# Kernel tuning notes

Measured on AMD Instinct MI355X. Metric: run time of the kernel, lower is better.

Reference implementation:

```python
import jax, jax.numpy as jnp
import numpy as np

NEG_SLOPE = 0.2
MASK_FILL = -1e9


def setup_inputs() -> dict:
    key = jax.random.key(0)
    k1, k2, k3, k4 = jax.random.split(key, 4)
    B, N, IN_DIM = 4, 2048, 256
    H, D = 8, 64  # n_heads, hidden_dim (out_dim)
    nodes = jax.random.normal(k1, (B, N, IN_DIM), dtype=jnp.float32)
    edges = jax.random.randint(k2, (B, N, N), 0, 2, dtype=jnp.int32)
    # Xavier-uniform-ish init for params
    pw_lim = float(np.sqrt(6.0 / (IN_DIM + H * D)))
    proj_weights = jax.random.uniform(k3, (IN_DIM, H * D), dtype=jnp.float32,
                                      minval=-pw_lim, maxval=pw_lim)
    aw_lim = float(np.sqrt(6.0 / (H + 2 * D)))
    attn_weights = jax.random.uniform(k4, (H, 2 * D), dtype=jnp.float32,
                                      minval=-aw_lim, maxval=aw_lim)
    return {"nodes": nodes, "edges": edges,
            "proj_weights": proj_weights, "attn_weights": attn_weights}


def reference(nodes, edges, proj_weights, attn_weights):
    B, N, _ = nodes.shape
    H, twoD = attn_weights.shape
    D = twoD // 2
    # Projection: [B,N,in] @ [in,H*D] -> [B,H,N,D]
    mapped = jnp.matmul(nodes, proj_weights).reshape(B, N, H, D).transpose(0, 2, 1, 3)
    # The left@diag(a)@right^T trick is exactly a_l.h_i + a_r.h_j:
    a_l = attn_weights[:, :D]   # [H,D]
    a_r = attn_weights[:, D:]   # [H,D]
    el = jnp.einsum('bhnd,hd->bhn', mapped, a_l)  # score contribution of source i
    er = jnp.einsum('bhnd,hd->bhn', mapped, a_r)  # score contribution of target j
    scores = jax.nn.leaky_relu(el[:, :, :, None] + er[:, :, None, :],
                               negative_slope=NEG_SLOPE)  # [B,H,N,N]
    scores = jnp.where(edges[:, None, :, :] == 0, MASK_FILL, scores)
    attn = jax.nn.softmax(scores, axis=-1)  # dropout p=0 -> identity
    out = jnp.einsum('bhij,bhjd->bhid', attn, mapped)  # [B,H,N,D]
    out = out.transpose(0, 2, 1, 3).reshape(B, N, H * D)  # is_concat=True
    return jax.nn.sigmoid(out)
```

## Files before the change

kernel.cpp:

```cpp
#include <hip/hip_runtime.h>
#include <hip/hip_fp16.h>
#include <math.h>

#define NEG 0.2f
#define LOG2E 1.4426950408889634f

typedef float f32x4 __attribute__((ext_vector_type(4)));
typedef _Float16 half8 __attribute__((ext_vector_type(8)));
typedef _Float16 h2v __attribute__((ext_vector_type(2)));
typedef short s16x2 __attribute__((ext_vector_type(2)));

#if __has_builtin(__builtin_amdgcn_exp2f)
#define EXP2F(x) __builtin_amdgcn_exp2f(x)
#else
#define EXP2F(x) exp2f(x)
#endif

__device__ inline uint cvt2(float a, float b) {
  union {
    decltype(__builtin_amdgcn_cvt_pkrtz(0.f, 0.f)) v;
    uint u;
  } x;
  x.v = __builtin_amdgcn_cvt_pkrtz(a, b);
  return x.u;
}

__device__ inline h2v u2h(uint u) {
  union {
    uint u;
    h2v v;
  } x;
  x.u = u;
  return x.v;
}

__device__ inline uint h2u(h2v v) {
  union {
    uint u;
    h2v v;
  } x;
  x.v = v;
  return x.u;
}

__device__ inline uint sgn16(uint t) {
  union {
    uint u;
    s16x2 v;
  } x;
  x.u = t;
  x.v = x.v >> 15;
  return x.u;
}


__global__ __launch_bounds__(256, 4) void prep_pack(
    const float* __restrict__ W, ushort* __restrict__ wf, uint* __restrict__ ermx,
    const int* __restrict__ e, uint* __restrict__ epk32) {
  const int bx = blockIdx.x;
  const int t = threadIdx.x;
  const int l = t & 63;
  if (bx < 33) {
    if (bx == 32) {
      if (t < 32) ermx[t] = 0u;
      return;
    }
    const int h = bx >> 2, ct = bx & 3;
#pragma unroll
    for (int s = 0; s < 2; ++s) {
      int slot = t + s * 256;
      int ll = slot & 63, kk = slot >> 6;
      int col = h * 64 + ct * 16 + (ll & 15);
      int k0 = kk * 32 + (ll >> 4) * 8;
      uint outv[4];
#pragma unroll
      for (int c = 0; c < 4; ++c) {
        float x0 = W[(size_t)(k0 + 2 * c) * 512 + col];
        float x1 = W[(size_t)(k0 + 2 * c + 1) * 512 + col];
        outv[c] = cvt2(x0, x1);
      }
      *(uint4*)&wf[(((size_t)((h * 4 + ct) * 8 + kk)) * 64 + ll) * 8] = *(uint4*)outv;
    }
    return;
  }
  const size_t g0 = (size_t)(bx - 33) * 16 + (t >> 6) * 4;
#pragma unroll
  for (int it = 0; it < 4; ++it) {
    const size_t gi = g0 + it;
    int4 v = *(const int4*)(e + gi * 256 + l * 4);
    unsigned long long b0 = __ballot(v.x != 0);
    unsigned long long b1 = __ballot(v.y != 0);
    unsigned long long b2 = __ballot(v.z != 0);
    unsigned long long b3 = __ballot(v.w != 0);
    if (l == 0) {
      uint4 lo, hi;
      lo.x = (uint)b0;
      lo.y = (uint)b1;
      lo.z = (uint)b2;
      lo.w = (uint)b3;
      hi.x = (uint)(b0 >> 32);
      hi.y = (uint)(b1 >> 32);
      hi.z = (uint)(b2 >> 32);
      hi.w = (uint)(b3 >> 32);
      *(uint4*)&epk32[gi * 8] = lo;
      *(uint4*)&epk32[gi * 8 + 4] = hi;
    }
  }
}

__global__ __launch_bounds__(256, 4) void pack2_proj(
    const int* __restrict__ e, uint* __restrict__ epk32,
    const float* __restrict__ A, const ushort* __restrict__ wf,
    const float* __restrict__ aw, ushort* __restrict__ mt,
    float* __restrict__ el, float* __restrict__ er, uint* __restrict__ ermx) {
  __shared__ ushort ct_lds[64][72];
  const int bx = blockIdx.x;
  const int t = threadIdx.x;
  const int l = t & 63;
  if (bx % 3 != 2) {
    const int pb = (bx / 3) * 2 + (bx % 3);
    const size_t g0 = 32768 + (size_t)pb * 16 + (t >> 6) * 4;
#pragma unroll
    for (int it = 0; it < 4; ++it) {
      const size_t gi = g0 + it;
      int4 v = *(const int4*)(e + gi * 256 + l * 4);
      unsigned long long b0 = __ballot(v.x != 0);
      unsigned long long b1 = __ballot(v.y != 0);
      unsigned long long b2 = __ballot(v.z != 0);
      unsigned long long b3 = __ballot(v.w != 0);
      if (l == 0) {
        uint4 lo, hi;
        lo.x = (uint)b0;
        lo.y = (uint)b1;
        lo.z = (uint)b2;
        lo.w = (uint)b3;
        hi.x = (uint)(b0 >> 32);
        hi.y = (uint)(b1 >> 32);
        hi.z = (uint)(b2 >> 32);
        hi.w = (uint)(b3 >> 32);
        *(uint4*)&epk32[gi * 8] = lo;
        *(uint4*)&epk32[gi * 8 + 4] = hi;
      }
    }
    return;
  }
  const int pid = bx / 3;
  const int wq = t >> 6;
  const int i0 = (pid & 127) * 64;
  const int h = pid >> 7;
  const int b = i0 >> 11, n0 = i0 & 2047, bh = b * 8 + h;
  const int cl = l & 15, hi = l >> 4;
  const float* arow = A + (size_t)(i0 + wq * 16 + cl) * 256 + hi * 8;
  const int4* wfb = (const int4*)wf + (size_t)h * 32 * 64 + l;
  f32x4 acc[4];
#pragma unroll
  for (int ct = 0; ct < 4; ++ct) acc[ct] = (f32x4){0.f, 0.f, 0.f, 0.f};
#pragma unroll
  for (int kk = 0; kk < 8; ++kk) {
    float4 a0 = *(const float4*)(arow + kk * 32);
    float4 a1 = *(const float4*)(arow + kk * 32 + 4);
    union {
      uint u[4];
      half8 v;
    } af;
    af.u[0] = cvt2(a0.x, a0.y);
    af.u[1] = cvt2(a0.z, a0.w);
    af.u[2] = cvt2(a1.x, a1.y);
    af.u[3] = cvt2(a1.z, a1.w);
#pragma unroll
    for (int ct = 0; ct < 4; ++ct) {
      union {
        int4 i;
        half8 v;
      } bf;
      bf.i = wfb[((size_t)ct * 8 + kk) * 64];
      acc[ct] = __builtin_amdgcn_mfma_f32_16x16x32_f16(af.v, bf.v, acc[ct], 0, 0, 0);
    }
  }
  float alc[4], arc[4];
#pragma unroll
  for (int ct = 0; ct < 4; ++ct) {
    alc[ct] = aw[h * 128 + ct * 16 + cl];
    arc[ct] = aw[h * 128 + 64 + ct * 16 + cl];
  }
  float ermax_loc = -1e30f;
#pragma unroll
  for (int reg = 0; reg < 4; ++reg) {
    float pl = acc[0][reg] * alc[0] + acc[1][reg] * alc[1] + acc[2][reg] * alc[2] +
               acc[3][reg] * alc[3];
    float pr = acc[0][reg] * arc[0] + acc[1][reg] * arc[1] + acc[2][reg] * arc[2] +
               acc[3][reg] * arc[3];
#pragma unroll
    for (int s = 1; s < 16; s <<= 1) {
      pl += __shfl_xor(pl, s);
      pr += __shfl_xor(pr, s);
    }
    if (cl == 0) {
      int n = n0 + wq * 16 + hi * 4 + reg;
      el[(size_t)bh * 2048 + n] = pl;
      er[(size_t)bh * 2048 + n] = pr;
    }
    ermax_loc = fmaxf(ermax_loc, pr);
  }
  ermax_loc = fmaxf(ermax_loc, __shfl_xor(ermax_loc, 16));
  ermax_loc = fmaxf(ermax_loc, __shfl_xor(ermax_loc, 32));
  if (l == 0) {
    uint bits = __float_as_uint(ermax_loc);
    uint key = (bits & 0x80000000u) ? ~bits : (bits | 0x80000000u);
    atomicMax(&ermx[bh], key);
  }
#pragma unroll
  for (int ct = 0; ct < 4; ++ct) {
    ushort4 us;
    us.x = __half_as_ushort(__float2half(acc[ct][0]));
    us.y = __half_as_ushort(__float2half(acc[ct][1]));
    us.z = __half_as_ushort(__float2half(acc[ct][2]));
    us.w = __half_as_ushort(__float2half(acc[ct][3]));
    *(ushort4*)&ct_lds[ct * 16 + cl][wq * 16 + hi * 4] = us;
  }
  __syncthreads();
  {
    const int f = t >> 5, s = t & 31;
    const int g = f >> 2, nt = f & 3;
    const int r = nt * 16 + (s & 15);
    const int cm = g * 32 + (s >> 4) * 8;
    int4 v0 = *(const int4*)&ct_lds[r][cm];
    int4 v1 = *(const int4*)&ct_lds[r][cm + 16];
    const size_t base = ((size_t)bh * 32 + (n0 >> 6)) * 4096 + f * 512;
    *(int4*)&mt[base + s * 8] = v0;
    *(int4*)&mt[base + (s + 32) * 8] = v1;
  }
}

__global__ __launch_bounds__(512, 4) void gat_attn(
    const ushort* __restrict__ mt, const uint* __restrict__ epk32,
    const float* __restrict__ el, const float* __restrict__ er,
    const uint* __restrict__ ermx, float* __restrict__ out) {
  __shared__ __align__(16) char smem[40960];
  int4* vt4 = (int4*)smem;
  uint* ysh = (uint*)(smem + 32768);
  uint* vsh = (uint*)(smem + 36864);
  const int t = threadIdx.x;
  const int l = t & 63;
  const int hf = t >> 8;
  const int th = t & 255;
  const int wq = (t >> 6) & 3;
  const int r16 = l & 15, hi = l >> 4;
  const int i0 = blockIdx.x * 64;
  const int h = blockIdx.y, b = blockIdx.z;
  const int bh = b * 8 + h;
  const uint ky = ermx[bh];
  const float emx = __uint_as_float((ky & 0x80000000u) ? (ky ^ 0x80000000u) : ~ky);
  {
    float4 e0 = *(const float4*)&er[(size_t)bh * 2048 + t * 4];
    uint2 yp, vp;
    yp.x = cvt2(EXP2F((e0.x - emx) * LOG2E), EXP2F((e0.y - emx) * LOG2E));
    yp.y = cvt2(EXP2F((e0.z - emx) * LOG2E), EXP2F((e0.w - emx) * LOG2E));
    vp.x = cvt2(EXP2F((e0.x - emx) * (NEG * LOG2E)), EXP2F((e0.y - emx) * (NEG * LOG2E)));
    vp.y = cvt2(EXP2F((e0.z - emx) * (NEG * LOG2E)), EXP2F((e0.w - emx) * (NEG * LOG2E)));
    *(uint2*)&ysh[t * 2] = yp;
    *(uint2*)&vsh[t * 2] = vp;
  }
  const int irow = i0 + wq * 16 + r16;
  h2v X2, U2;
  {
    const float s0 = el[(size_t)bh * 2048 + irow] + emx;
    const float m2 = fmaxf(s0, NEG * s0) * LOG2E;
    const float Xf = EXP2F(s0 * LOG2E - m2);
    const float Uf = EXP2F(NEG * s0 * LOG2E - m2);
    X2 = u2h(cvt2(Xf, Xf));
    U2 = u2h(cvt2(Uf, Uf));
  }
  const uint* prow = epk32 + (size_t)(b * 2048 + irow) * 64 + hf * 32;
  f32x4 acc[4];
  f32x4 accL = {0.f, 0.f, 0.f, 0.f};
#pragma unroll
  for (int nt = 0; nt < 4; ++nt) acc[nt] = (f32x4){0.f, 0.f, 0.f, 0.f};
  half8 ones;
#pragma unroll
  for (int c = 0; c < 8; ++c) ones[c] = (_Float16)1.f;

  const int4* srcbase = (const int4*)mt + ((size_t)bh * 32 + hf * 16) * 512 + wq * 128 + l;
  uint4 epw = *(const uint4*)&prow[0];
  {
    int4 p0 = srcbase[0];
    int4 p1 = srcbase[64];
    int4* d = vt4 + hf * 512 + wq * 128 + l;
    d[0] = p0;
    d[64] = p1;
  }
  __syncthreads();
  int cur = 0;
  for (int jt = 0; jt < 16; ++jt) {
    int4 nx0, nx1;
    uint4 epwn;
    if (jt < 15) {
      const int4* s = srcbase + (size_t)(jt + 1) * 512;
      nx0 = s[0];
      nx1 = s[64];
      const int jn = jt + 1;
      epwn = *(const uint4*)&prow[((jn >> 2) << 3) + (((jn >> 1) & 1) << 2)];
    }
    half8 af[2];
#pragma unroll
    for (int g = 0; g < 2; ++g) {
      const uint idx = (hf * 16 + jt) * 32 + g * 16 + hi * 4;
      uint4 y4 = *(const uint4*)&ysh[idx];
      uint4 v4 = *(const uint4*)&vsh[idx];
      const uint bsh = ((jt & 1) << 4) + (g << 3) + hi * 2;
      const uint p0 = epw.x >> bsh, p1 = epw.y >> bsh;
      const uint p2 = epw.z >> bsh, p3 = epw.w >> bsh;
      union {
        uint u[4];
        half8 v8;
      } fr;
      fr.u[0] = h2u(__builtin_elementwise_max(X2 * u2h(y4.x), U2 * u2h(v4.x))) &
                sgn16(((p0 & 1u) << 15) | (p1 << 31));
      fr.u[1] = h2u(__builtin_elementwise_max(X2 * u2h(y4.y), U2 * u2h(v4.y))) &
                sgn16(((p2 & 1u) << 15) | (p3 << 31));
      fr.u[2] = h2u(__builtin_elementwise_max(X2 * u2h(y4.z), U2 * u2h(v4.z))) &
                sgn16((((p0 >> 1) & 1u) << 15) | ((p1 >> 1) << 31));
      fr.u[3] = h2u(__builtin_elementwise_max(X2 * u2h(y4.w), U2 * u2h(v4.w))) &
                sgn16((((p2 >> 1) & 1u) << 15) | ((p3 >> 1) << 31));
      af[g] = fr.v8;
    }
    const half8* fb = (const half8*)(vt4 + cur * 1024 + hf * 512);
    __builtin_amdgcn_s_setprio(1);
#pragma unroll
    for (int g = 0; g < 2; ++g) {
      accL = __builtin_amdgcn_mfma_f32_16x16x32_f16(af[g], ones, accL, 0, 0, 0);
#pragma unroll
      for (int nt = 0; nt < 4; ++nt) {
        half8 bfr = fb[(g * 4 + nt) * 64 + l];
        acc[nt] = __builtin_amdgcn_mfma_f32_16x16x32_f16(af[g], bfr, acc[nt], 0, 0, 0);
      }
    }
    __builtin_amdgcn_s_setprio(0);
    if (jt < 15) {
      int4* d = vt4 + (cur ^ 1) * 1024 + hf * 512 + wq * 128 + l;
      d[0] = nx0;
      d[64] = nx1;
      epw = epwn;
    }
    __syncthreads();
    cur ^= 1;
  }
  float* red = (float*)smem;
  if (hf == 1) {
    float* dst = red + th * 21;
#pragma unroll
    for (int nt = 0; nt < 4; ++nt)
#pragma unroll
      for (int k = 0; k < 4; ++k) dst[nt * 4 + k] = acc[nt][k];
#pragma unroll
    for (int k = 0; k < 4; ++k) dst[16 + k] = accL[k];
  }
  __syncthreads();
  if (hf == 0) {
    const float* src = red + th * 21;
#pragma unroll
    for (int reg = 0; reg < 4; ++reg) {
      float Lrow = accL[reg] + src[16 + reg];
      float invL = 1.f / Lrow;
      int orow = i0 + wq * 16 + hi * 4 + reg;
#pragma unroll
      for (int nt = 0; nt < 4; ++nt) {
        float o = (acc[nt][reg] + src[nt * 4 + reg]) * invL;
        float sig = 1.f / (1.f + __expf(-o));
        out[(size_t)(b * 2048 + orow) * 512 + h * 64 + nt * 16 + r16] = sig;
      }
    }
  }
}

extern "C" void kernel_launch(void* const* d_in, const int* in_sizes, int n_in,
                              void* d_out, int out_size, void* d_ws, size_t ws_size,
                              hipStream_t stream) {
  const float* nodes = (const float*)d_in[0];
  const int* edges = (const int*)d_in[1];
  const float* pw = (const float*)d_in[2];
  const float* aw = (const float*)d_in[3];
  float* out = (float*)d_out;

  ushort* mt = (ushort*)d_ws;
  float* el = (float*)((char*)d_ws + 8388608);
  float* er = (float*)((char*)d_ws + 8650752);
  uint* ermx = (uint*)((char*)d_ws + 8912896);
  uint* epk = (uint*)((char*)d_ws + 8913024);
  ushort* wf = (ushort*)((char*)d_ws + 11010176);

  prep_pack<<<2081, 256, 0, stream>>>(pw, wf, ermx, edges, epk);
  pack2_proj<<<3072, 256, 0, stream>>>(edges, epk, nodes, wf, aw, mt, el, er, ermx);
  gat_attn<<<dim3(32, 8, 4), 512, 0, stream>>>(mt, epk, el, er, ermx, out);
}
```

Before: 88.18 us.

## Load V fragments directly from global and remap block order for L2 locality

Removes the double-buffered LDS staging of the projected value tiles: each wave now loads its MFMA B-fragments straight from global memory into registers every iteration, dropping the per-iteration __syncthreads and shrinking shared memory. The grid is flattened to 1D with a swizzled block index so consecutive blocks are spread across (b,h) groups, likely to improve cache or XCD locality. The trade-off is exposed global-load latency without explicit prefetch and higher register use.

```diff
diff --git a/kernel.cpp b/kernel.cpp
--- a/kernel.cpp
+++ b/kernel.cpp
@@ -236,18 +236,18 @@
     const ushort* __restrict__ mt, const uint* __restrict__ epk32,
     const float* __restrict__ el, const float* __restrict__ er,
     const uint* __restrict__ ermx, float* __restrict__ out) {
-  __shared__ __align__(16) char smem[40960];
-  int4* vt4 = (int4*)smem;
-  uint* ysh = (uint*)(smem + 32768);
-  uint* vsh = (uint*)(smem + 36864);
+  __shared__ __align__(16) char smem[29696];
+  uint* ysh = (uint*)(smem + 21504);
+  uint* vsh = (uint*)(smem + 25600);
   const int t = threadIdx.x;
   const int l = t & 63;
   const int hf = t >> 8;
   const int th = t & 255;
   const int wq = (t >> 6) & 3;
   const int r16 = l & 15, hi = l >> 4;
-  const int i0 = blockIdx.x * 64;
-  const int h = blockIdx.y, b = blockIdx.z;
+  const int nb = (blockIdx.x & 7) * 128 + (blockIdx.x >> 3);
+  const int i0 = (nb & 31) * 64;
+  const int h = (nb >> 5) & 7, b = nb >> 8;
   const int bh = b * 8 + h;
   const uint ky = ermx[bh];
   const float emx = __uint_as_float((ky & 0x80000000u) ? (ky ^ 0x80000000u) : ~ky);
@@ -280,27 +280,14 @@
 #pragma unroll
   for (int c = 0; c < 8; ++c) ones[c] = (_Float16)1.f;
 
-  const int4* srcbase = (const int4*)mt + ((size_t)bh * 32 + hf * 16) * 512 + wq * 128 + l;
-  uint4 epw = *(const uint4*)&prow[0];
-  {
-    int4 p0 = srcbase[0];
-    int4 p1 = srcbase[64];
-    int4* d = vt4 + hf * 512 + wq * 128 + l;
-    d[0] = p0;
-    d[64] = p1;
-  }
+  const half8* vbase = (const half8*)mt + ((size_t)bh * 32 + hf * 16) * 512 + l;
   __syncthreads();
-  int cur = 0;
   for (int jt = 0; jt < 16; ++jt) {
-    int4 nx0, nx1;
-    uint4 epwn;
-    if (jt < 15) {
-      const int4* s = srcbase + (size_t)(jt + 1) * 512;
-      nx0 = s[0];
-      nx1 = s[64];
-      const int jn = jt + 1;
-      epwn = *(const uint4*)&prow[((jn >> 2) << 3) + (((jn >> 1) & 1) << 2)];
-    }
+    const half8* vt_ptr = vbase + (size_t)jt * 512;
+    half8 vf[8];
+#pragma unroll
+    for (int f = 0; f < 8; ++f) vf[f] = vt_ptr[f * 64];
+    const uint4 epw = *(const uint4*)&prow[((jt >> 2) << 3) + (((jt >> 1) & 1) << 2)];
     half8 af[2];
 #pragma unroll
     for (int g = 0; g < 2; ++g) {
@@ -324,27 +311,18 @@
                 sgn16((((p2 >> 1) & 1u) << 15) | ((p3 >> 1) << 31));
       af[g] = fr.v8;
     }
-    const half8* fb = (const half8*)(vt4 + cur * 1024 + hf * 512);
     __builtin_amdgcn_s_setprio(1);
 #pragma unroll
     for (int g = 0; g < 2; ++g) {
       accL = __builtin_amdgcn_mfma_f32_16x16x32_f16(af[g], ones, accL, 0, 0, 0);
 #pragma unroll
       for (int nt = 0; nt < 4; ++nt) {
-        half8 bfr = fb[(g * 4 + nt) * 64 + l];
-        acc[nt] = __builtin_amdgcn_mfma_f32_16x16x32_f16(af[g], bfr, acc[nt], 0, 0, 0);
+        acc[nt] = __builtin_amdgcn_mfma_f32_16x16x32_f16(af[g], vf[g * 4 + nt], acc[nt], 0, 0, 0);
       }
     }
     __builtin_amdgcn_s_setprio(0);
-    if (jt < 15) {
-      int4* d = vt4 + (cur ^ 1) * 1024 + hf * 512 + wq * 128 + l;
-      d[0] = nx0;
-      d[64] = nx1;
-      epw = epwn;
-    }
-    __syncthreads();
-    cur ^= 1;
-  }
+  }
+  __syncthreads();
   float* red = (float*)smem;
   if (hf == 1) {
     float* dst = red + th * 21;
@@ -391,5 +369,5 @@
 
   prep_pack<<<2081, 256, 0, stream>>>(pw, wf, ermx, edges, epk);
   pack2_proj<<<3072, 256, 0, stream>>>(edges, epk, nodes, wf, aw, mt, el, er, ermx);
-  gat_attn<<<dim3(32, 8, 4), 512, 0, stream>>>(mt, epk, el, er, ermx, out);
-}
+  gat_attn<<<1024, 512, 0, stream>>>(mt, epk, el, er, ermx, out);
+}
```

After: 97.42 us. +10.5%, slower.

## Drop split-K halves in attention kernel; one 256-thread block covers all keys

Applied to the files above, without the earlier changes.

The attention kernel previously split the key dimension across two 256-thread halves of a 512-thread block, then reduced the partial accumulators through LDS. Now each 256-thread block walks all 32 key tiles serially, which removes the cross-half reduction and its extra barrier and shrinks shared memory. The cost is half as many threads per block and a longer serial loop per wave, so there is less latency hiding unless occupancy from the smaller LDS footprint makes up for it.

```diff
diff --git a/kernel.cpp b/kernel.cpp
--- a/kernel.cpp
+++ b/kernel.cpp
@@ -232,19 +232,17 @@
   }
 }
 
-__global__ __launch_bounds__(512, 4) void gat_attn(
+__global__ __launch_bounds__(256, 4) void gat_attn(
     const ushort* __restrict__ mt, const uint* __restrict__ epk32,
     const float* __restrict__ el, const float* __restrict__ er,
     const uint* __restrict__ ermx, float* __restrict__ out) {
-  __shared__ __align__(16) char smem[40960];
+  __shared__ __align__(16) char smem[24576];
   int4* vt4 = (int4*)smem;
-  uint* ysh = (uint*)(smem + 32768);
-  uint* vsh = (uint*)(smem + 36864);
+  uint* ysh = (uint*)(smem + 16384);
+  uint* vsh = (uint*)(smem + 20480);
   const int t = threadIdx.x;
   const int l = t & 63;
-  const int hf = t >> 8;
-  const int th = t & 255;
-  const int wq = (t >> 6) & 3;
+  const int wq = t >> 6;
   const int r16 = l & 15, hi = l >> 4;
   const int i0 = blockIdx.x * 64;
   const int h = blockIdx.y, b = blockIdx.z;
@@ -252,14 +250,19 @@
   const uint ky = ermx[bh];
   const float emx = __uint_as_float((ky & 0x80000000u) ? (ky ^ 0x80000000u) : ~ky);
   {
-    float4 e0 = *(const float4*)&er[(size_t)bh * 2048 + t * 4];
-    uint2 yp, vp;
+    float4 e0 = *(const float4*)&er[(size_t)bh * 2048 + t * 8];
+    float4 e1 = *(const float4*)&er[(size_t)bh * 2048 + t * 8 + 4];
+    uint4 yp, vp;
     yp.x = cvt2(EXP2F((e0.x - emx) * LOG2E), EXP2F((e0.y - emx) * LOG2E));
     yp.y = cvt2(EXP2F((e0.z - emx) * LOG2E), EXP2F((e0.w - emx) * LOG2E));
+    yp.z = cvt2(EXP2F((e1.x - emx) * LOG2E), EXP2F((e1.y - emx) * LOG2E));
+    yp.w = cvt2(EXP2F((e1.z - emx) * LOG2E), EXP2F((e1.w - emx) * LOG2E));
     vp.x = cvt2(EXP2F((e0.x - emx) * (NEG * LOG2E)), EXP2F((e0.y - emx) * (NEG * LOG2E)));
     vp.y = cvt2(EXP2F((e0.z - emx) * (NEG * LOG2E)), EXP2F((e0.w - emx) * (NEG * LOG2E)));
-    *(uint2*)&ysh[t * 2] = yp;
-    *(uint2*)&vsh[t * 2] = vp;
+    vp.z = cvt2(EXP2F((e1.x - emx) * (NEG * LOG2E)), EXP2F((e1.y - emx) * (NEG * LOG2E)));
+    vp.w = cvt2(EXP2F((e1.z - emx) * (NEG * LOG2E)), EXP2F((e1.w - emx) * (NEG * LOG2E)));
+    *(uint4*)&ysh[t * 4] = yp;
+    *(uint4*)&vsh[t * 4] = vp;
   }
   const int irow = i0 + wq * 16 + r16;
   h2v X2, U2;
@@ -271,7 +274,7 @@
     X2 = u2h(cvt2(Xf, Xf));
     U2 = u2h(cvt2(Uf, Uf));
   }
-  const uint* prow = epk32 + (size_t)(b * 2048 + irow) * 64 + hf * 32;
+  const uint* prow = epk32 + (size_t)(b * 2048 + irow) * 64;
   f32x4 acc[4];
   f32x4 accL = {0.f, 0.f, 0.f, 0.f};
 #pragma unroll
@@ -280,21 +283,21 @@
 #pragma unroll
   for (int c = 0; c < 8; ++c) ones[c] = (_Float16)1.f;
 
-  const int4* srcbase = (const int4*)mt + ((size_t)bh * 32 + hf * 16) * 512 + wq * 128 + l;
+  const int4* srcbase = (const int4*)mt + (size_t)bh * 32 * 512 + wq * 128 + l;
   uint4 epw = *(const uint4*)&prow[0];
   {
     int4 p0 = srcbase[0];
     int4 p1 = srcbase[64];
-    int4* d = vt4 + hf * 512 + wq * 128 + l;
+    int4* d = vt4 + wq * 128 + l;
     d[0] = p0;
     d[64] = p1;
   }
   __syncthreads();
   int cur = 0;
-  for (int jt = 0; jt < 16; ++jt) {
+  for (int jt = 0; jt < 32; ++jt) {
     int4 nx0, nx1;
     uint4 epwn;
-    if (jt < 15) {
+    if (jt < 31) {
       const int4* s = srcbase + (size_t)(jt + 1) * 512;
       nx0 = s[0];
       nx1 = s[64];
@@ -304,7 +307,7 @@
     half8 af[2];
 #pragma unroll
     for (int g = 0; g < 2; ++g) {
-      const uint idx = (hf * 16 + jt) * 32 + g * 16 + hi * 4;
+      const uint idx = jt * 32 + g * 16 + hi * 4;
       uint4 y4 = *(const uint4*)&ysh[idx];
       uint4 v4 = *(const uint4*)&vsh[idx];
       const uint bsh = ((jt & 1) << 4) + (g << 3) + hi * 2;
@@ -324,7 +327,7 @@
                 sgn16((((p2 >> 1) & 1u) << 15) | ((p3 >> 1) << 31));
       af[g] = fr.v8;
     }
-    const half8* fb = (const half8*)(vt4 + cur * 1024 + hf * 512);
+    const half8* fb = (const half8*)(vt4 + cur * 512);
     __builtin_amdgcn_s_setprio(1);
 #pragma unroll
     for (int g = 0; g < 2; ++g) {
@@ -336,8 +339,8 @@
       }
     }
     __builtin_amdgcn_s_setprio(0);
-    if (jt < 15) {
-      int4* d = vt4 + (cur ^ 1) * 1024 + hf * 512 + wq * 128 + l;
+    if (jt < 31) {
+      int4* d = vt4 + (cur ^ 1) * 512 + wq * 128 + l;
       d[0] = nx0;
       d[64] = nx1;
       epw = epwn;
@@ -345,30 +348,15 @@
     __syncthreads();
     cur ^= 1;
   }
-  float* red = (float*)smem;
-  if (hf == 1) {
-    float* dst = red + th * 21;
-#pragma unroll
-    for (int nt = 0; nt < 4; ++nt)
-#pragma unroll
-      for (int k = 0; k < 4; ++k) dst[nt * 4 + k] = acc[nt][k];
-#pragma unroll
-    for (int k = 0; k < 4; ++k) dst[16 + k] = accL[k];
-  }
-  __syncthreads();
-  if (hf == 0) {
-    const float* src = red + th * 21;
-#pragma unroll
-    for (int reg = 0; reg < 4; ++reg) {
-      float Lrow = accL[reg] + src[16 + reg];
-      float invL = 1.f / Lrow;
-      int orow = i0 + wq * 16 + hi * 4 + reg;
-#pragma unroll
-      for (int nt = 0; nt < 4; ++nt) {
-        float o = (acc[nt][reg] + src[nt * 4 + reg]) * invL;
-        float sig = 1.f / (1.f + __expf(-o));
-        out[(size_t)(b * 2048 + orow) * 512 + h * 64 + nt * 16 + r16] = sig;
-      }
+#pragma unroll
+  for (int reg = 0; reg < 4; ++reg) {
+    float invL = 1.f / accL[reg];
+    int orow = i0 + wq * 16 + hi * 4 + reg;
+#pragma unroll
+    for (int nt = 0; nt < 4; ++nt) {
+      float o = acc[nt][reg] * invL;
+      float sig = 1.f / (1.f + __expf(-o));
+      out[(size_t)(b * 2048 + orow) * 512 + h * 64 + nt * 16 + r16] = sig;
     }
   }
 }
@@ -391,5 +379,5 @@
 
   prep_pack<<<2081, 256, 0, stream>>>(pw, wf, ermx, edges, epk);
   pack2_proj<<<3072, 256, 0, stream>>>(edges, epk, nodes, wf, aw, mt, el, er, ermx);
-  gat_attn<<<dim3(32, 8, 4), 512, 0, stream>>>(mt, epk, el, er, ermx, out);
-}
+  gat_attn<<<dim3(32, 8, 4), 256, 0, stream>>>(mt, epk, el, er, ermx, out);
+}
```

Result: no change. 87.40 us (-0.9%).
